# Optimization experiments

Hardware: AMD Instinct MI355X
Metric: run time of the kernel (lower is better)

The kernel has to match this reference:

```python
import jax, jax.numpy as jnp
import numpy as np

NORM_S = 3.0  # normalize_scale, learn_scale=False
NUM_CLASSES = 32


def setup_inputs() -> dict:
    key = jax.random.key(0)
    k1, k2 = jax.random.split(key)
    x = jax.random.normal(k1, (512, 128), dtype=jnp.float32)
    labels = jax.random.randint(k2, (512,), 0, NUM_CLASSES, dtype=jnp.int64)
    return {"x": x, "labels": labels}


def reference(x, labels):
    # L2-normalize rows and scale (MyTripletLoss.forward)
    f = NORM_S * x / jnp.linalg.norm(x, axis=1, keepdims=True)
    # pairwise squared distances, clamped at 0 (pairwise_distances)
    sq = jnp.sum(f * f, axis=1)
    D = jnp.clip(sq[:, None] + sq[None, :] - 2.0 * (f @ f.T), 0.0, None)  # [N,N]
    N = x.shape[0]
    # triplet_type == 0: valid triplet (i,j,k) iff i!=j, l_i==l_j, l_i!=l_k
    same = (labels[:, None] == labels[None, :]) & (~jnp.eye(N, dtype=bool))  # [i,j]
    diff = labels[:, None] != labels[None, :]                                # [i,k]
    mask = same[:, :, None] & diff[:, None, :]                               # [i,j,k]
    # DBL loss: log(1 + exp(D_ij - D_ik)) = softplus
    lt = jax.nn.softplus(D[:, :, None] - D[:, None, :])                      # [i,j,k]
    triplet_count = jnp.sum(mask).astype(lt.dtype)
    loss = jnp.sum(jnp.where(mask, lt, 0.0)) / triplet_count
    return loss.reshape(1)
```

## Files before the change

### kernel.cpp

```cpp
#include <hip/hip_runtime.h>
#include <math.h>

#define N 512
#define DIM 128
#define NORM_S 3.0f
#define TR 64
#define PADS 132


__global__ void __launch_bounds__(256) triplet_kernel(const float* __restrict__ x,
                                                      const int* __restrict__ labels,
                                                      float* __restrict__ sums,
                                                      float* __restrict__ cnts) {
    __shared__ float xt[TR * PADS];
    __shared__ float xi[DIM];
    __shared__ int   lab[N];
    __shared__ float sameD[N];
    __shared__ float diffD[N];
    __shared__ float red[256];
    __shared__ float rni_sh;
    __shared__ int   nsame, ndiff;

    int i = blockIdx.x;
    int t = threadIdx.x;

    if (t < DIM) xi[t] = x[i * DIM + t];
    for (int j = t; j < N; j += 256) lab[j] = labels[j];
    if (t == 0) { nsame = 0; ndiff = 0; }
    __syncthreads();

    red[t] = (t < DIM) ? xi[t] * xi[t] : 0.0f;
    __syncthreads();
    #pragma unroll
    for (int s = 128; s > 0; s >>= 1) {
        if (t < s) red[t] += red[t + s];
        __syncthreads();
    }
    if (t == 0) rni_sh = rsqrtf(red[0]);
    __syncthreads();

    int li  = lab[i];
    float rni = rni_sh;
    int quart = t & 3;
    int jloc  = t >> 2;
    int dbase = quart * 32;

    float4 bx[8];
    {
        const float4* b = (const float4*)(xi + dbase);
        #pragma unroll
        for (int q = 0; q < 8; ++q) bx[q] = b[q];
    }

    for (int tile = 0; tile < N / TR; ++tile) {
        int base = tile * TR;
        const float4* src = (const float4*)(x + base * DIM);
        #pragma unroll
        for (int k = 0; k < (TR * DIM / 4) / 256; ++k) {
            int e  = t + k * 256;
            int r  = e >> 5;
            int c4 = e & 31;
            float4 v = src[e];
            *((float4*)(xt + r * PADS + 4 * c4)) = v;
        }
        __syncthreads();

        float dsum, ssum;
        {
            const float4* a = (const float4*)(xt + jloc * PADS + dbase);
            float d0 = 0.0f, d1 = 0.0f, s0 = 0.0f, s1 = 0.0f;
            #pragma unroll
            for (int q = 0; q < 8; q += 2) {
                float4 a0 = a[q + 0];
                float4 a1 = a[q + 1];
                d0 += a0.x * bx[q].x + a0.y * bx[q].y + a0.z * bx[q].z + a0.w * bx[q].w;
                d1 += a1.x * bx[q + 1].x + a1.y * bx[q + 1].y + a1.z * bx[q + 1].z + a1.w * bx[q + 1].w;
                s0 += a0.x * a0.x + a0.y * a0.y + a0.z * a0.z + a0.w * a0.w;
                s1 += a1.x * a1.x + a1.y * a1.y + a1.z * a1.z + a1.w * a1.w;
            }
            dsum = d0 + d1;
            ssum = s0 + s1;
        }
        dsum += __shfl_xor(dsum, 1, 64);
        dsum += __shfl_xor(dsum, 2, 64);
        ssum += __shfl_xor(ssum, 1, 64);
        ssum += __shfl_xor(ssum, 2, 64);

        if (quart == 0) {
            float rnj = rsqrtf(ssum);
            int j = base + jloc;
            float D = 18.0f * fmaxf(0.0f, 1.0f - dsum * rni * rnj);
            int lj = lab[j];
            if (lj == li) {
                if (j != i) { int p = atomicAdd(&nsame, 1); sameD[p] = D; }
            } else {
                int p = atomicAdd(&ndiff, 1); diffD[p] = D;
            }
        }
        __syncthreads();
    }

    int ns = nsame, nd = ndiff;
    float lsum = 0.0f;
    for (int js = 0; js < ns; ++js) {
        float Dij = sameD[js];
        for (int ks = t; ks < nd; ks += 256) {
            float d = Dij - diffD[ks];
            lsum += __logf(1.0f + __expf(d));
        }
    }

    red[t] = lsum;
    __syncthreads();
    #pragma unroll
    for (int s = 128; s > 0; s >>= 1) {
        if (t < s) red[t] += red[t + s];
        __syncthreads();
    }
    if (t == 0) {
        sums[i] = red[0];
        cnts[i] = (float)(ns * nd);
    }
}

__global__ void __launch_bounds__(256) finalize_kernel(const float* __restrict__ sums,
                                                       const float* __restrict__ cnts,
                                                       float* __restrict__ out) {
    __shared__ float2 red[256];
    int t = threadIdx.x;
    float2 v;
    v.x = sums[t] + sums[t + 256];
    v.y = cnts[t] + cnts[t + 256];
    red[t] = v;
    __syncthreads();
    #pragma unroll
    for (int s = 128; s > 0; s >>= 1) {
        if (t < s) {
            red[t].x += red[t + s].x;
            red[t].y += red[t + s].y;
        }
        __syncthreads();
    }
    if (t == 0) out[0] = red[0].x / red[0].y;
}

extern "C" void kernel_launch(void* const* d_in, const int* in_sizes, int n_in,
                              void* d_out, int out_size, void* d_ws, size_t ws_size,
                              hipStream_t stream) {
    const float* x      = (const float*)d_in[0];
    const int*   labels = (const int*)d_in[1];
    float*       out    = (float*)d_out;

    float* sums = (float*)d_ws;
    float* cnts = sums + N;

    triplet_kernel<<<N, 256, 0, stream>>>(x, labels, sums, cnts);
    finalize_kernel<<<1, 256, 0, stream>>>(sums, cnts, out);
}
```

Measured before the change: 72.92 us.

## Factor softplus exponentials, widen blocks to 512 threads, defer distance classification

```diff
diff --git a/kernel.cpp b/kernel.cpp
--- a/kernel.cpp
+++ b/kernel.cpp
@@ -3,61 +3,48 @@
 
 #define N 512
 #define DIM 128
-#define NORM_S 3.0f
-#define TR 64
+#define TR 128
 #define PADS 132
+#define BT 512
 
 
-__global__ void __launch_bounds__(256) triplet_kernel(const float* __restrict__ x,
-                                                      const int* __restrict__ labels,
-                                                      float* __restrict__ sums,
-                                                      float* __restrict__ cnts) {
+__global__ void __launch_bounds__(BT) triplet_kernel(const float* __restrict__ x,
+                                                     const int* __restrict__ labels,
+                                                     float* __restrict__ sums,
+                                                     float* __restrict__ cnts) {
     __shared__ float xt[TR * PADS];
-    __shared__ float xi[DIM];
     __shared__ int   lab[N];
+    __shared__ float dotv[N];
+    __shared__ float ssqv[N];
     __shared__ float sameD[N];
     __shared__ float diffD[N];
-    __shared__ float red[256];
-    __shared__ float rni_sh;
+    __shared__ float red[BT / 64];
     __shared__ int   nsame, ndiff;
 
     int i = blockIdx.x;
     int t = threadIdx.x;
 
-    if (t < DIM) xi[t] = x[i * DIM + t];
-    for (int j = t; j < N; j += 256) lab[j] = labels[j];
+    lab[t] = labels[t];
     if (t == 0) { nsame = 0; ndiff = 0; }
-    __syncthreads();
 
-    red[t] = (t < DIM) ? xi[t] * xi[t] : 0.0f;
-    __syncthreads();
-    #pragma unroll
-    for (int s = 128; s > 0; s >>= 1) {
-        if (t < s) red[t] += red[t + s];
-        __syncthreads();
-    }
-    if (t == 0) rni_sh = rsqrtf(red[0]);
-    __syncthreads();
-
-    int li  = lab[i];
-    float rni = rni_sh;
     int quart = t & 3;
     int jloc  = t >> 2;
     int dbase = quart * 32;
 
     float4 bx[8];
     {
-        const float4* b = (const float4*)(xi + dbase);
+        const float4* b = (const float4*)(x + i * DIM + dbase);
         #pragma unroll
         for (int q = 0; q < 8; ++q) bx[q] = b[q];
     }
+    __syncthreads();
 
     for (int tile = 0; tile < N / TR; ++tile) {
         int base = tile * TR;
         const float4* src = (const float4*)(x + base * DIM);
         #pragma unroll
-        for (int k = 0; k < (TR * DIM / 4) / 256; ++k) {
-            int e  = t + k * 256;
+        for (int k = 0; k < (TR * DIM / 4) / BT; ++k) {
+            int e  = t + k * BT;
             int r  = e >> 5;
             int c4 = e & 31;
             float4 v = src[e];
@@ -65,60 +52,63 @@
         }
         __syncthreads();
 
-        float dsum, ssum;
-        {
-            const float4* a = (const float4*)(xt + jloc * PADS + dbase);
-            float d0 = 0.0f, d1 = 0.0f, s0 = 0.0f, s1 = 0.0f;
-            #pragma unroll
-            for (int q = 0; q < 8; q += 2) {
-                float4 a0 = a[q + 0];
-                float4 a1 = a[q + 1];
-                d0 += a0.x * bx[q].x + a0.y * bx[q].y + a0.z * bx[q].z + a0.w * bx[q].w;
-                d1 += a1.x * bx[q + 1].x + a1.y * bx[q + 1].y + a1.z * bx[q + 1].z + a1.w * bx[q + 1].w;
-                s0 += a0.x * a0.x + a0.y * a0.y + a0.z * a0.z + a0.w * a0.w;
-                s1 += a1.x * a1.x + a1.y * a1.y + a1.z * a1.z + a1.w * a1.w;
-            }
-            dsum = d0 + d1;
-            ssum = s0 + s1;
+        const float4* a = (const float4*)(xt + jloc * PADS + dbase);
+        float d0 = 0.0f, d1 = 0.0f, s0 = 0.0f, s1 = 0.0f;
+        #pragma unroll
+        for (int q = 0; q < 8; q += 2) {
+            float4 a0 = a[q + 0];
+            float4 a1 = a[q + 1];
+            d0 += a0.x * bx[q].x + a0.y * bx[q].y + a0.z * bx[q].z + a0.w * bx[q].w;
+            d1 += a1.x * bx[q + 1].x + a1.y * bx[q + 1].y + a1.z * bx[q + 1].z + a1.w * bx[q + 1].w;
+            s0 += a0.x * a0.x + a0.y * a0.y + a0.z * a0.z + a0.w * a0.w;
+            s1 += a1.x * a1.x + a1.y * a1.y + a1.z * a1.z + a1.w * a1.w;
         }
+        float dsum = d0 + d1;
+        float ssum = s0 + s1;
         dsum += __shfl_xor(dsum, 1, 64);
         dsum += __shfl_xor(dsum, 2, 64);
         ssum += __shfl_xor(ssum, 1, 64);
         ssum += __shfl_xor(ssum, 2, 64);
-
         if (quart == 0) {
-            float rnj = rsqrtf(ssum);
-            int j = base + jloc;
-            float D = 18.0f * fmaxf(0.0f, 1.0f - dsum * rni * rnj);
-            int lj = lab[j];
-            if (lj == li) {
-                if (j != i) { int p = atomicAdd(&nsame, 1); sameD[p] = D; }
-            } else {
-                int p = atomicAdd(&ndiff, 1); diffD[p] = D;
-            }
+            dotv[base + jloc] = dsum;
+            ssqv[base + jloc] = ssum;
         }
         __syncthreads();
     }
 
-    int ns = nsame, nd = ndiff;
-    float lsum = 0.0f;
-    for (int js = 0; js < ns; ++js) {
-        float Dij = sameD[js];
-        for (int ks = t; ks < nd; ks += 256) {
-            float d = Dij - diffD[ks];
-            lsum += __logf(1.0f + __expf(d));
+    {
+        float rni = rsqrtf(ssqv[i]);
+        int j = t;
+        float D = 18.0f * fmaxf(0.0f, 1.0f - dotv[j] * rsqrtf(ssqv[j]) * rni);
+        int li = lab[i];
+        if (lab[j] == li) {
+            if (j != i) { int p = atomicAdd(&nsame, 1); sameD[p] = D; }
+        } else {
+            int p = atomicAdd(&ndiff, 1); diffD[p] = D;
         }
     }
+    __syncthreads();
 
-    red[t] = lsum;
+    int ns = nsame, nd = ndiff;
+    float ek = (t < nd) ? __expf(-diffD[t]) : 0.0f;
+    float lsum = 0.0f;
+    float snext = (ns > 0) ? sameD[0] : 0.0f;
+    for (int js = 0; js < ns; ++js) {
+        float ds = snext;
+        snext = sameD[js + 1];
+        float es = __expf(ds);
+        lsum += __logf(1.0f + es * ek);
+    }
+
+    #pragma unroll
+    for (int off = 32; off > 0; off >>= 1) lsum += __shfl_xor(lsum, off, 64);
+    if ((t & 63) == 0) red[t >> 6] = lsum;
     __syncthreads();
-    #pragma unroll
-    for (int s = 128; s > 0; s >>= 1) {
-        if (t < s) red[t] += red[t + s];
-        __syncthreads();
-    }
     if (t == 0) {
-        sums[i] = red[0];
+        float s = 0.0f;
+        #pragma unroll
+        for (int w = 0; w < BT / 64; ++w) s += red[w];
+        sums[i] = s;
         cnts[i] = (float)(ns * nd);
     }
 }
@@ -154,6 +144,6 @@
     float* sums = (float*)d_ws;
     float* cnts = sums + N;
 
-    triplet_kernel<<<N, 256, 0, stream>>>(x, labels, sums, cnts);
+    triplet_kernel<<<N, BT, 0, stream>>>(x, labels, sums, cnts);
     finalize_kernel<<<1, 256, 0, stream>>>(sums, cnts, out);
 }
```

Result: faster. 71.11 us (-2.5%).
